# Performance work log

Hardware: AMD Instinct MI355X
Metric: run time of the kernel (lower is better)

## Reference

```python
import jax, jax.numpy as jnp
import numpy as np

N, OBS, H, M, L = 512, 32, 128, 128, 3


def _w(key, shape, fan_in):
    return jax.random.normal(key, shape, dtype=jnp.float32) / np.sqrt(fan_in)


def setup_inputs() -> dict:
    key = jax.random.key(0)
    ks = iter(jax.random.split(key, 64))
    inp = {}
    inp["obs"] = jax.random.normal(next(ks), (N, OBS), dtype=jnp.float32)
    inp["pos"] = jax.random.uniform(next(ks), (N, 2), dtype=jnp.float32)
    # encoder: obs_dim -> H -> H -> H
    inp["enc_W1"] = _w(next(ks), (H, OBS), OBS); inp["enc_b1"] = jnp.zeros((H,), jnp.float32)
    inp["enc_W2"] = _w(next(ks), (H, H), H);     inp["enc_b2"] = jnp.zeros((H,), jnp.float32)
    inp["enc_W3"] = _w(next(ks), (H, H), H);     inp["enc_b3"] = jnp.zeros((H,), jnp.float32)
    # per-layer message MLPs: (2H+1) -> M -> M -> M, stacked over L layers
    inp["msg_W1"] = _w(next(ks), (L, M, 2 * H + 1), 2 * H + 1); inp["msg_b1"] = jnp.zeros((L, M), jnp.float32)
    inp["msg_W2"] = _w(next(ks), (L, M, M), M);                 inp["msg_b2"] = jnp.zeros((L, M), jnp.float32)
    inp["msg_W3"] = _w(next(ks), (L, M, M), M);                 inp["msg_b3"] = jnp.zeros((L, M), jnp.float32)
    # per-layer update MLPs: (H+M) -> H -> H -> H, stacked over L layers
    inp["upd_W1"] = _w(next(ks), (L, H, H + M), H + M); inp["upd_b1"] = jnp.zeros((L, H), jnp.float32)
    inp["upd_W2"] = _w(next(ks), (L, H, H), H);         inp["upd_b2"] = jnp.zeros((L, H), jnp.float32)
    inp["upd_W3"] = _w(next(ks), (L, H, H), H);         inp["upd_b3"] = jnp.zeros((L, H), jnp.float32)
    return inp


def _mlp3(x, W1, b1, W2, b2, W3, b3):
    h = jax.nn.relu(x @ W1.T + b1)
    h = jax.nn.relu(h @ W2.T + b2)
    return h @ W3.T + b3


def reference(obs, pos, enc_W1, enc_b1, enc_W2, enc_b2, enc_W3, enc_b3,
              msg_W1, msg_b1, msg_W2, msg_b2, msg_W3, msg_b3,
              upd_W1, upd_b1, upd_W2, upd_b2, upd_W3, upd_b3):
    n = obs.shape[0]
    h = enc_W1.shape[0]
    z = _mlp3(obs, enc_W1, enc_b1, enc_W2, enc_b2, enc_W3, enc_b3)  # (N, H)
    # pairwise distances; guard diagonal sqrt(0) for grad safety, then zero it
    diff = pos[:, None, :] - pos[None, :, :]                  # (N, N, 2)
    sq = jnp.sum(diff * diff, axis=-1)                        # (N, N)
    eye = jnp.eye(n, dtype=pos.dtype)
    dist = jnp.sqrt(jnp.where(eye > 0, 1.0, sq)) * (1.0 - eye)
    nondiag = (1.0 - eye)[:, :, None]
    n_layers = msg_W1.shape[0]
    for l in range(n_layers):
        W1 = msg_W1[l]
        Wi, Wj, wd = W1[:, :h], W1[:, h:2 * h], W1[:, 2 * h]  # split concat [z_i, z_j, d]
        A = z @ Wi.T                                          # (N, M) receiver term
        B = z @ Wj.T                                          # (N, M) sender term
        h1 = jax.nn.relu(A[:, None, :] + B[None, :, :] + dist[:, :, None] * wd + msg_b1[l])  # (N, N, M)
        h2 = jax.nn.relu(jnp.einsum('ijm,km->ijk', h1, msg_W2[l]) + msg_b2[l])
        m = jnp.einsum('ijm,km->ijk', h2, msg_W3[l]) + msg_b3[l]
        m = m * nondiag                                       # exclude j == i
        msum = jnp.sum(m, axis=1)                             # (N, M) sum over senders j
        z = _mlp3(jnp.concatenate([z, msum], axis=-1),
                  upd_W1[l], upd_b1[l], upd_W2[l], upd_b2[l], upd_W3[l], upd_b3[l])
    return z
```

## Files before the change

kernel.cpp:

```cpp
#include <hip/hip_runtime.h>

#define NA 512
#define NOBS 32
#define NH 128

typedef const float* fp32p;
typedef __attribute__((ext_vector_type(8))) short bf16x8;
typedef __attribute__((ext_vector_type(4))) float f32x4;

__device__ __forceinline__ short f2bf(float f) {
    union { float f; unsigned u; } v; v.f = f;
    unsigned r = v.u + 0x7fffu + ((v.u >> 16) & 1u);
    return (short)(r >> 16);
}

__device__ __forceinline__ bf16x8 wfrag_f4(const float* p) {
    float4 u = *(const float4*)p;
    float4 v = *(const float4*)(p + 4);
    bf16x8 f;
    f[0] = f2bf(u.x); f[1] = f2bf(u.y); f[2] = f2bf(u.z); f[3] = f2bf(u.w);
    f[4] = f2bf(v.x); f[5] = f2bf(v.y); f[6] = f2bf(v.z); f[7] = f2bf(v.w);
    return f;
}

#define HSTR 136

__global__ __launch_bounds__(512) void enc_ab_kernel(
    fp32p obs, fp32p eW1, fp32p eb1, fp32p eW2, fp32p eb2, fp32p eW3, fp32p eb3,
    fp32p mW1, float* __restrict__ z, float* __restrict__ A, float* __restrict__ B) {
    const int i = blockIdx.x;
    const int t = threadIdx.x;
    const int nn = t >> 2;
    const int ks = t & 3;

    __shared__ float xs0[NOBS];
    __shared__ float part[4 * NH];
    __shared__ float part2[4 * NH];
    __shared__ float hx[NH], hy[NH], zz[NH];

    if (t < NOBS) xs0[t] = obs[(size_t)i * NOBS + t];
    __syncthreads();
    {
        const float* wr = eW1 + (size_t)nn * NOBS + ks * 8;
        const float4 w0 = *(const float4*)wr;
        const float4 w1 = *(const float4*)(wr + 4);
        const float4 x0 = *(const float4*)&xs0[ks * 8];
        const float4 x1 = *(const float4*)&xs0[ks * 8 + 4];
        part[ks * NH + nn] = w0.x * x0.x + w0.y * x0.y + w0.z * x0.z + w0.w * x0.w +
                             w1.x * x1.x + w1.y * x1.y + w1.z * x1.z + w1.w * x1.w;
    }
    __syncthreads();
    if (t < NH)
        hx[t] = fmaxf(eb1[t] + part[t] + part[NH + t] + part[2 * NH + t] + part[3 * NH + t], 0.f);
    __syncthreads();
    {
        const float* wr = eW2 + (size_t)nn * NH + ks * 4;
        float p = 0.f;
        #pragma unroll
        for (int it = 0; it < 8; ++it) {
            const float4 wv = *(const float4*)(wr + it * 16);
            const float4 xv = *(const float4*)&hx[it * 16 + ks * 4];
            p += wv.x * xv.x + wv.y * xv.y + wv.z * xv.z + wv.w * xv.w;
        }
        part[ks * NH + nn] = p;
    }
    __syncthreads();
    if (t < NH)
        hy[t] = fmaxf(eb2[t] + part[t] + part[NH + t] + part[2 * NH + t] + part[3 * NH + t], 0.f);
    __syncthreads();
    {
        const float* wr = eW3 + (size_t)nn * NH + ks * 4;
        float p = 0.f;
        #pragma unroll
        for (int it = 0; it < 8; ++it) {
            const float4 wv = *(const float4*)(wr + it * 16);
            const float4 xv = *(const float4*)&hy[it * 16 + ks * 4];
            p += wv.x * xv.x + wv.y * xv.y + wv.z * xv.z + wv.w * xv.w;
        }
        part[ks * NH + nn] = p;
    }
    __syncthreads();
    if (t < NH) {
        const float v = eb3[t] + part[t] + part[NH + t] + part[2 * NH + t] + part[3 * NH + t];
        z[(size_t)i * NH + t] = v;
        zz[t] = v;
    }
    __syncthreads();
    {
        const float* pr = mW1 + (size_t)nn * 257;
        float pa = 0.f, pb = 0.f;
        #pragma unroll
        for (int it = 0; it < 8; ++it) {
            #pragma unroll
            for (int j = 0; j < 4; ++j) {
                const int k = it * 16 + ks * 4 + j;
                const float x = zz[k];
                pa += x * pr[k];
                pb += x * pr[NH + k];
            }
        }
        part[ks * NH + nn] = pa;
        part2[ks * NH + nn] = pb;
    }
    __syncthreads();
    if (t < NH) {
        A[(size_t)i * NH + t] = part[t] + part[NH + t] + part[2 * NH + t] + part[3 * NH + t];
        B[(size_t)i * NH + t] = part2[t] + part2[NH + t] + part2[2 * NH + t] + part2[3 * NH + t];
    }
}

__global__ __launch_bounds__(512) void msg_upd_kernel(
    const float* __restrict__ A, const float* __restrict__ B,
    fp32p pos, const float* __restrict__ zin,
    fp32p W1l, fp32p b1, fp32p W2, fp32p b2, fp32p W3, fp32p b3,
    fp32p uW1, fp32p ub1, fp32p uW2, fp32p ub2, fp32p uW3, fp32p ub3,
    fp32p msgW1n, int do_ab,
    float* __restrict__ zout, float* __restrict__ An, float* __restrict__ Bn) {
    const int i = blockIdx.x;
    const int t = threadIdx.x;
    const int lane = t & 63;
    const int w = t >> 6;
    const int q = lane >> 4;
    const int c = lane & 15;
    const int ncol = w * 16 + c;

    __shared__ short h1s[128 * HSTR];
    __shared__ short h2s[128 * HSTR];
    __shared__ float distrow[NA];
    __shared__ float amrow[NH];
    __shared__ float wdsr[NH];
    __shared__ float xs2[2 * NH];
    __shared__ float part[4 * NH];
    __shared__ float part2[4 * NH];
    __shared__ float hx[NH], hy[NH], hz[NH];

    if (t < NH) {
        amrow[t] = A[i * NH + t] + b1[t];
        wdsr[t]  = W1l[t * 257 + 256];
        xs2[t] = zin[(size_t)i * NH + t];
    }
    {
        const float2 pi = *(const float2*)&pos[2 * i];
        const float2 pj = *(const float2*)&pos[2 * t];
        const float dx = pi.x - pj.x, dy = pi.y - pj.y;
        const float s = dx * dx + dy * dy;
        distrow[t] = (t == i) ? 0.0f : sqrtf(s);
    }

    bf16x8 w2f[4], w3f[4];
    {
        const float* w2r = W2 + (size_t)ncol * NH + q * 8;
        const float* w3r = W3 + (size_t)ncol * NH + q * 8;
        #pragma unroll
        for (int kb = 0; kb < 4; ++kb) {
            w2f[kb] = wfrag_f4(w2r + kb * 32);
            w3f[kb] = wfrag_f4(w3r + kb * 32);
        }
    }
    const float b2n = b2[ncol];
    const float b3n = b3[ncol];

    const int m2 = lane * 2;
    float psum = 0.0f;

    for (int c4 = 0; c4 < 4; ++c4) {
        const int j0 = c4 * 128;
        __syncthreads();

        {
            const float am0 = amrow[m2],     am1 = amrow[m2 + 1];
            const float wd0 = wdsr[m2],      wd1 = wdsr[m2 + 1];
            #pragma unroll
            for (int rr = 0; rr < 16; ++rr) {
                const int row = rr * 8 + w;
                const int jg  = j0 + row;
                const float2 bv = *(const float2*)&B[(size_t)jg * NH + m2];
                const float d = distrow[jg];
                const float v0 = fmaxf(am0 + bv.x + d * wd0, 0.0f);
                const float v1 = fmaxf(am1 + bv.y + d * wd1, 0.0f);
                const unsigned p = (unsigned)(unsigned short)f2bf(v0) |
                                   ((unsigned)(unsigned short)f2bf(v1) << 16);
                *(unsigned*)&h1s[row * HSTR + m2] = p;
            }
        }
        __syncthreads();

        #pragma unroll
        for (int jt = 0; jt < 8; ++jt) {
            f32x4 acc = {0.f, 0.f, 0.f, 0.f};
            const short* arow = &h1s[(jt * 16 + c) * HSTR + q * 8];
            #pragma unroll
            for (int kb = 0; kb < 4; ++kb) {
                bf16x8 a = *(const bf16x8*)(arow + kb * 32);
                acc = __builtin_amdgcn_mfma_f32_16x16x32_bf16(a, w2f[kb], acc, 0, 0, 0);
            }
            #pragma unroll
            for (int r = 0; r < 4; ++r) {
                const int row = jt * 16 + q * 4 + r;
                h2s[row * HSTR + ncol] = f2bf(fmaxf(acc[r] + b2n, 0.0f));
            }
        }
        __syncthreads();

        #pragma unroll
        for (int jt = 0; jt < 8; ++jt) {
            f32x4 acc = {0.f, 0.f, 0.f, 0.f};
            const short* arow = &h2s[(jt * 16 + c) * HSTR + q * 8];
            #pragma unroll
            for (int kb = 0; kb < 4; ++kb) {
                bf16x8 a = *(const bf16x8*)(arow + kb * 32);
                acc = __builtin_amdgcn_mfma_f32_16x16x32_bf16(a, w3f[kb], acc, 0, 0, 0);
            }
            #pragma unroll
            for (int r = 0; r < 4; ++r) {
                const int jg = j0 + jt * 16 + q * 4 + r;
                if (jg != i) psum += acc[r] + b3n;
            }
        }
    }

    psum += __shfl_xor(psum, 16, 64);
    psum += __shfl_xor(psum, 32, 64);
    if (lane < 16) xs2[NH + ncol] = psum;
    __syncthreads();

    const int nn = t >> 2;
    const int ks = t & 3;
    {
        const float* wr = uW1 + (size_t)nn * 256 + ks * 4;
        float p = 0.f;
        #pragma unroll
        for (int it = 0; it < 16; ++it) {
            const float4 wv = *(const float4*)(wr + it * 16);
            const float4 xv = *(const float4*)&xs2[it * 16 + ks * 4];
            p += wv.x * xv.x + wv.y * xv.y + wv.z * xv.z + wv.w * xv.w;
        }
        part[ks * NH + nn] = p;
    }
    __syncthreads();
    if (t < NH)
        hx[t] = fmaxf(ub1[t] + part[t] + part[NH + t] + part[2 * NH + t] + part[3 * NH + t], 0.f);
    __syncthreads();
    {
        const float* wr = uW2 + (size_t)nn * NH + ks * 4;
        float p = 0.f;
        #pragma unroll
        for (int it = 0; it < 8; ++it) {
            const float4 wv = *(const float4*)(wr + it * 16);
            const float4 xv = *(const float4*)&hx[it * 16 + ks * 4];
            p += wv.x * xv.x + wv.y * xv.y + wv.z * xv.z + wv.w * xv.w;
        }
        part[ks * NH + nn] = p;
    }
    __syncthreads();
    if (t < NH)
        hy[t] = fmaxf(ub2[t] + part[t] + part[NH + t] + part[2 * NH + t] + part[3 * NH + t], 0.f);
    __syncthreads();
    {
        const float* wr = uW3 + (size_t)nn * NH + ks * 4;
        float p = 0.f;
        #pragma unroll
        for (int it = 0; it < 8; ++it) {
            const float4 wv = *(const float4*)(wr + it * 16);
            const float4 xv = *(const float4*)&hy[it * 16 + ks * 4];
            p += wv.x * xv.x + wv.y * xv.y + wv.z * xv.z + wv.w * xv.w;
        }
        part[ks * NH + nn] = p;
    }
    __syncthreads();
    if (t < NH) {
        const float v = ub3[t] + part[t] + part[NH + t] + part[2 * NH + t] + part[3 * NH + t];
        zout[(size_t)i * NH + t] = v;
        hz[t] = v;
    }
    if (!do_ab) return;
    __syncthreads();
    {
        const float* pr = msgW1n + (size_t)nn * 257;
        float pa = 0.f, pb = 0.f;
        #pragma unroll
        for (int it = 0; it < 8; ++it) {
            #pragma unroll
            for (int j = 0; j < 4; ++j) {
                const int k = it * 16 + ks * 4 + j;
                const float x = hz[k];
                pa += x * pr[k];
                pb += x * pr[NH + k];
            }
        }
        part[ks * NH + nn] = pa;
        part2[ks * NH + nn] = pb;
    }
    __syncthreads();
    if (t < NH) {
        An[(size_t)i * NH + t] = part[t] + part[NH + t] + part[2 * NH + t] + part[3 * NH + t];
        Bn[(size_t)i * NH + t] = part2[t] + part2[NH + t] + part2[2 * NH + t] + part2[3 * NH + t];
    }
}

extern "C" void kernel_launch(void* const* d_in, const int* in_sizes, int n_in,
                              void* d_out, int out_size, void* d_ws, size_t ws_size,
                              hipStream_t stream) {
    fp32p obs   = (fp32p)d_in[0];
    fp32p pos   = (fp32p)d_in[1];
    fp32p encW1 = (fp32p)d_in[2];  fp32p encb1 = (fp32p)d_in[3];
    fp32p encW2 = (fp32p)d_in[4];  fp32p encb2 = (fp32p)d_in[5];
    fp32p encW3 = (fp32p)d_in[6];  fp32p encb3 = (fp32p)d_in[7];
    fp32p msgW1 = (fp32p)d_in[8];  fp32p msgb1 = (fp32p)d_in[9];
    fp32p msgW2 = (fp32p)d_in[10]; fp32p msgb2 = (fp32p)d_in[11];
    fp32p msgW3 = (fp32p)d_in[12]; fp32p msgb3 = (fp32p)d_in[13];
    fp32p updW1 = (fp32p)d_in[14]; fp32p updb1 = (fp32p)d_in[15];
    fp32p updW2 = (fp32p)d_in[16]; fp32p updb2 = (fp32p)d_in[17];
    fp32p updW3 = (fp32p)d_in[18]; fp32p updb3 = (fp32p)d_in[19];

    float* ws = (float*)d_ws;
    float* zA = ws;
    float* zB = zA + NA * NH;
    float* A0 = zB + NA * NH;
    float* B0 = A0 + NA * NH;
    float* A1 = B0 + NA * NH;
    float* B1 = A1 + NA * NH;

    enc_ab_kernel<<<NA, 512, 0, stream>>>(obs, encW1, encb1, encW2, encb2,
                                          encW3, encb3, msgW1, zA, A0, B0);

    float* zin = zA;  float* zout = zB;
    float* Ac = A0;   float* Bc = B0;
    float* An = A1;   float* Bn = B1;
    for (int l = 0; l < 3; ++l) {
        const int do_ab = (l < 2);
        float* dst = (l == 2) ? (float*)d_out : zout;
        msg_upd_kernel<<<NA, 512, 0, stream>>>(Ac, Bc, pos, zin,
            msgW1 + (size_t)l * 128 * 257, msgb1 + l * 128,
            msgW2 + (size_t)l * 128 * 128, msgb2 + l * 128,
            msgW3 + (size_t)l * 128 * 128, msgb3 + l * 128,
            updW1 + (size_t)l * 256 * 128, updb1 + l * 128,
            updW2 + (size_t)l * 128 * 128, updb2 + l * 128,
            updW3 + (size_t)l * 128 * 128, updb3 + l * 128,
            msgW1 + (size_t)(l + 1 < 3 ? l + 1 : 0) * 128 * 257, do_ab,
            dst, An, Bn);
        float* tmp;
        tmp = zin; zin = zout; zout = tmp;
        tmp = Ac; Ac = An; An = tmp;
        tmp = Bc; Bc = Bn; Bn = tmp;
    }
}
```

Baseline: 225.3 us.

## Fuse encoder and all message layers into one persistent kernel with grid barriers

Replaces the four separate kernel launches with a single persistent kernel that runs the encoder and all three message/update layers, using atomic-counter grid barriers between layers. The receiver term A and the node state z now stay in shared memory, and only B goes through global memory. The shared h1/h2 tiles shrink to 64 rows so that more blocks fit per CU and all 512 blocks can be co-resident. The barrier relies on every block being resident at once, so it could deadlock or serialise if occupancy is insufficient, and it adds spin-wait overhead.

```diff
diff --git a/kernel.cpp b/kernel.cpp
--- a/kernel.cpp
+++ b/kernel.cpp
@@ -25,19 +25,60 @@
 
 #define HSTR 136
 
-__global__ __launch_bounds__(512) void enc_ab_kernel(
-    fp32p obs, fp32p eW1, fp32p eb1, fp32p eW2, fp32p eb2, fp32p eW3, fp32p eb3,
-    fp32p mW1, float* __restrict__ z, float* __restrict__ A, float* __restrict__ B) {
+__device__ __forceinline__ void gsync(unsigned* cnt, int s) {
+    __threadfence();
+    __syncthreads();
+    if (threadIdx.x == 0) {
+        atomicAdd(&cnt[s], 1u);
+        while (__hip_atomic_load(&cnt[s], __ATOMIC_RELAXED,
+                                 __HIP_MEMORY_SCOPE_AGENT) < (unsigned)NA) {
+            __builtin_amdgcn_s_sleep(2);
+        }
+    }
+    __syncthreads();
+    (void)__hip_atomic_load(&cnt[s], __ATOMIC_ACQUIRE, __HIP_MEMORY_SCOPE_AGENT);
+}
+
+__global__ void init_kernel(unsigned* cnt) {
+    if (threadIdx.x < 8) cnt[threadIdx.x] = 0u;
+}
+
+__global__ __launch_bounds__(512) void gnn_kernel(
+    fp32p obs, fp32p pos,
+    fp32p eW1, fp32p eb1, fp32p eW2, fp32p eb2, fp32p eW3, fp32p eb3,
+    fp32p mW1, fp32p mb1, fp32p mW2, fp32p mb2, fp32p mW3, fp32p mb3,
+    fp32p uW1, fp32p ub1, fp32p uW2, fp32p ub2, fp32p uW3, fp32p ub3,
+    float* __restrict__ out, float* __restrict__ B0, float* __restrict__ B1,
+    unsigned* __restrict__ cnt) {
     const int i = blockIdx.x;
     const int t = threadIdx.x;
+    const int lane = t & 63;
+    const int w = t >> 6;
+    const int q = lane >> 4;
+    const int c = lane & 15;
+    const int ncol = w * 16 + c;
     const int nn = t >> 2;
     const int ks = t & 3;
 
-    __shared__ float xs0[NOBS];
+    __shared__ short h1s[64 * HSTR];
+    __shared__ short h2s[64 * HSTR];
+    __shared__ float distrow[NA];
+    __shared__ float amrow[NH];
+    __shared__ float wdsr[NH];
+    __shared__ float arow_s[NH];
+    __shared__ float xs2[2 * NH];
     __shared__ float part[4 * NH];
     __shared__ float part2[4 * NH];
-    __shared__ float hx[NH], hy[NH], zz[NH];
-
+    __shared__ float hx[NH], hy[NH];
+    __shared__ float xs0[NOBS];
+
+    {
+        const float2 pi = *(const float2*)&pos[2 * i];
+        const float2 pj = *(const float2*)&pos[2 * t];
+        const float dx = pi.x - pj.x, dy = pi.y - pj.y;
+        const float s = dx * dx + dy * dy;
+        distrow[t] = (t == i) ? 0.0f : sqrtf(s);
+    }
     if (t < NOBS) xs0[t] = obs[(size_t)i * NOBS + t];
     __syncthreads();
     {
@@ -80,11 +121,8 @@
         part[ks * NH + nn] = p;
     }
     __syncthreads();
-    if (t < NH) {
-        const float v = eb3[t] + part[t] + part[NH + t] + part[2 * NH + t] + part[3 * NH + t];
-        z[(size_t)i * NH + t] = v;
-        zz[t] = v;
-    }
+    if (t < NH)
+        xs2[t] = eb3[t] + part[t] + part[NH + t] + part[2 * NH + t] + part[3 * NH + t];
     __syncthreads();
     {
         const float* pr = mW1 + (size_t)nn * 257;
@@ -94,7 +132,7 @@
             #pragma unroll
             for (int j = 0; j < 4; ++j) {
                 const int k = it * 16 + ks * 4 + j;
-                const float x = zz[k];
+                const float x = xs2[k];
                 pa += x * pr[k];
                 pb += x * pr[NH + k];
             }
@@ -104,197 +142,181 @@
     }
     __syncthreads();
     if (t < NH) {
-        A[(size_t)i * NH + t] = part[t] + part[NH + t] + part[2 * NH + t] + part[3 * NH + t];
-        B[(size_t)i * NH + t] = part2[t] + part2[NH + t] + part2[2 * NH + t] + part2[3 * NH + t];
-    }
-}
-
-__global__ __launch_bounds__(512) void msg_upd_kernel(
-    const float* __restrict__ A, const float* __restrict__ B,
-    fp32p pos, const float* __restrict__ zin,
-    fp32p W1l, fp32p b1, fp32p W2, fp32p b2, fp32p W3, fp32p b3,
-    fp32p uW1, fp32p ub1, fp32p uW2, fp32p ub2, fp32p uW3, fp32p ub3,
-    fp32p msgW1n, int do_ab,
-    float* __restrict__ zout, float* __restrict__ An, float* __restrict__ Bn) {
-    const int i = blockIdx.x;
-    const int t = threadIdx.x;
-    const int lane = t & 63;
-    const int w = t >> 6;
-    const int q = lane >> 4;
-    const int c = lane & 15;
-    const int ncol = w * 16 + c;
-
-    __shared__ short h1s[128 * HSTR];
-    __shared__ short h2s[128 * HSTR];
-    __shared__ float distrow[NA];
-    __shared__ float amrow[NH];
-    __shared__ float wdsr[NH];
-    __shared__ float xs2[2 * NH];
-    __shared__ float part[4 * NH];
-    __shared__ float part2[4 * NH];
-    __shared__ float hx[NH], hy[NH], hz[NH];
-
-    if (t < NH) {
-        amrow[t] = A[i * NH + t] + b1[t];
-        wdsr[t]  = W1l[t * 257 + 256];
-        xs2[t] = zin[(size_t)i * NH + t];
-    }
-    {
-        const float2 pi = *(const float2*)&pos[2 * i];
-        const float2 pj = *(const float2*)&pos[2 * t];
-        const float dx = pi.x - pj.x, dy = pi.y - pj.y;
-        const float s = dx * dx + dy * dy;
-        distrow[t] = (t == i) ? 0.0f : sqrtf(s);
-    }
-
-    bf16x8 w2f[4], w3f[4];
-    {
-        const float* w2r = W2 + (size_t)ncol * NH + q * 8;
-        const float* w3r = W3 + (size_t)ncol * NH + q * 8;
-        #pragma unroll
-        for (int kb = 0; kb < 4; ++kb) {
-            w2f[kb] = wfrag_f4(w2r + kb * 32);
-            w3f[kb] = wfrag_f4(w3r + kb * 32);
-        }
-    }
-    const float b2n = b2[ncol];
-    const float b3n = b3[ncol];
-
-    const int m2 = lane * 2;
-    float psum = 0.0f;
-
-    for (int c4 = 0; c4 < 4; ++c4) {
-        const int j0 = c4 * 128;
-        __syncthreads();
-
+        arow_s[t] = part[t] + part[NH + t] + part[2 * NH + t] + part[3 * NH + t];
+        B0[(size_t)i * NH + t] = part2[t] + part2[NH + t] + part2[2 * NH + t] + part2[3 * NH + t];
+    }
+    gsync(cnt, 0);
+
+    for (int l = 0; l < 3; ++l) {
+        const float* Bc = (l == 1) ? B1 : B0;
+        float* Bn = (l == 0) ? B1 : B0;
+        fp32p W1l = mW1 + (size_t)l * 128 * 257;
+        fp32p b1l = mb1 + l * 128;
+        fp32p W2l = mW2 + (size_t)l * 128 * 128;
+        fp32p b2l = mb2 + l * 128;
+        fp32p W3l = mW3 + (size_t)l * 128 * 128;
+        fp32p b3l = mb3 + l * 128;
+        fp32p uW1l = uW1 + (size_t)l * 256 * 128;
+        fp32p ub1l = ub1 + l * 128;
+        fp32p uW2l = uW2 + (size_t)l * 128 * 128;
+        fp32p ub2l = ub2 + l * 128;
+        fp32p uW3l = uW3 + (size_t)l * 128 * 128;
+        fp32p ub3l = ub3 + l * 128;
+
+        if (t < NH) {
+            amrow[t] = arow_s[t] + b1l[t];
+            wdsr[t]  = W1l[t * 257 + 256];
+        }
+        bf16x8 w2f[4], w3f[4];
         {
-            const float am0 = amrow[m2],     am1 = amrow[m2 + 1];
-            const float wd0 = wdsr[m2],      wd1 = wdsr[m2 + 1];
-            #pragma unroll
-            for (int rr = 0; rr < 16; ++rr) {
-                const int row = rr * 8 + w;
-                const int jg  = j0 + row;
-                const float2 bv = *(const float2*)&B[(size_t)jg * NH + m2];
-                const float d = distrow[jg];
-                const float v0 = fmaxf(am0 + bv.x + d * wd0, 0.0f);
-                const float v1 = fmaxf(am1 + bv.y + d * wd1, 0.0f);
-                const unsigned p = (unsigned)(unsigned short)f2bf(v0) |
-                                   ((unsigned)(unsigned short)f2bf(v1) << 16);
-                *(unsigned*)&h1s[row * HSTR + m2] = p;
-            }
-        }
-        __syncthreads();
-
-        #pragma unroll
-        for (int jt = 0; jt < 8; ++jt) {
-            f32x4 acc = {0.f, 0.f, 0.f, 0.f};
-            const short* arow = &h1s[(jt * 16 + c) * HSTR + q * 8];
+            const float* w2r = W2l + (size_t)ncol * NH + q * 8;
+            const float* w3r = W3l + (size_t)ncol * NH + q * 8;
             #pragma unroll
             for (int kb = 0; kb < 4; ++kb) {
-                bf16x8 a = *(const bf16x8*)(arow + kb * 32);
-                acc = __builtin_amdgcn_mfma_f32_16x16x32_bf16(a, w2f[kb], acc, 0, 0, 0);
-            }
-            #pragma unroll
-            for (int r = 0; r < 4; ++r) {
-                const int row = jt * 16 + q * 4 + r;
-                h2s[row * HSTR + ncol] = f2bf(fmaxf(acc[r] + b2n, 0.0f));
-            }
-        }
-        __syncthreads();
-
-        #pragma unroll
-        for (int jt = 0; jt < 8; ++jt) {
-            f32x4 acc = {0.f, 0.f, 0.f, 0.f};
-            const short* arow = &h2s[(jt * 16 + c) * HSTR + q * 8];
-            #pragma unroll
-            for (int kb = 0; kb < 4; ++kb) {
-                bf16x8 a = *(const bf16x8*)(arow + kb * 32);
-                acc = __builtin_amdgcn_mfma_f32_16x16x32_bf16(a, w3f[kb], acc, 0, 0, 0);
-            }
-            #pragma unroll
-            for (int r = 0; r < 4; ++r) {
-                const int jg = j0 + jt * 16 + q * 4 + r;
-                if (jg != i) psum += acc[r] + b3n;
-            }
-        }
-    }
-
-    psum += __shfl_xor(psum, 16, 64);
-    psum += __shfl_xor(psum, 32, 64);
-    if (lane < 16) xs2[NH + ncol] = psum;
-    __syncthreads();
-
-    const int nn = t >> 2;
-    const int ks = t & 3;
-    {
-        const float* wr = uW1 + (size_t)nn * 256 + ks * 4;
-        float p = 0.f;
-        #pragma unroll
-        for (int it = 0; it < 16; ++it) {
-            const float4 wv = *(const float4*)(wr + it * 16);
-            const float4 xv = *(const float4*)&xs2[it * 16 + ks * 4];
-            p += wv.x * xv.x + wv.y * xv.y + wv.z * xv.z + wv.w * xv.w;
-        }
-        part[ks * NH + nn] = p;
-    }
-    __syncthreads();
-    if (t < NH)
-        hx[t] = fmaxf(ub1[t] + part[t] + part[NH + t] + part[2 * NH + t] + part[3 * NH + t], 0.f);
-    __syncthreads();
-    {
-        const float* wr = uW2 + (size_t)nn * NH + ks * 4;
-        float p = 0.f;
-        #pragma unroll
-        for (int it = 0; it < 8; ++it) {
-            const float4 wv = *(const float4*)(wr + it * 16);
-            const float4 xv = *(const float4*)&hx[it * 16 + ks * 4];
-            p += wv.x * xv.x + wv.y * xv.y + wv.z * xv.z + wv.w * xv.w;
-        }
-        part[ks * NH + nn] = p;
-    }
-    __syncthreads();
-    if (t < NH)
-        hy[t] = fmaxf(ub2[t] + part[t] + part[NH + t] + part[2 * NH + t] + part[3 * NH + t], 0.f);
-    __syncthreads();
-    {
-        const float* wr = uW3 + (size_t)nn * NH + ks * 4;
-        float p = 0.f;
-        #pragma unroll
-        for (int it = 0; it < 8; ++it) {
-            const float4 wv = *(const float4*)(wr + it * 16);
-            const float4 xv = *(const float4*)&hy[it * 16 + ks * 4];
-            p += wv.x * xv.x + wv.y * xv.y + wv.z * xv.z + wv.w * xv.w;
-        }
-        part[ks * NH + nn] = p;
-    }
-    __syncthreads();
-    if (t < NH) {
-        const float v = ub3[t] + part[t] + part[NH + t] + part[2 * NH + t] + part[3 * NH + t];
-        zout[(size_t)i * NH + t] = v;
-        hz[t] = v;
-    }
-    if (!do_ab) return;
-    __syncthreads();
-    {
-        const float* pr = msgW1n + (size_t)nn * 257;
-        float pa = 0.f, pb = 0.f;
-        #pragma unroll
-        for (int it = 0; it < 8; ++it) {
-            #pragma unroll
-            for (int j = 0; j < 4; ++j) {
-                const int k = it * 16 + ks * 4 + j;
-                const float x = hz[k];
-                pa += x * pr[k];
-                pb += x * pr[NH + k];
-            }
-        }
-        part[ks * NH + nn] = pa;
-        part2[ks * NH + nn] = pb;
-    }
-    __syncthreads();
-    if (t < NH) {
-        An[(size_t)i * NH + t] = part[t] + part[NH + t] + part[2 * NH + t] + part[3 * NH + t];
-        Bn[(size_t)i * NH + t] = part2[t] + part2[NH + t] + part2[2 * NH + t] + part2[3 * NH + t];
+                w2f[kb] = wfrag_f4(w2r + kb * 32);
+                w3f[kb] = wfrag_f4(w3r + kb * 32);
+            }
+        }
+        const float b2n = b2l[ncol];
+        const float b3n = b3l[ncol];
+
+        const int m2 = lane * 2;
+        float psum = 0.0f;
+
+        for (int c8 = 0; c8 < 8; ++c8) {
+            const int j0 = c8 * 64;
+            __syncthreads();
+
+            {
+                const float am0 = amrow[m2],     am1 = amrow[m2 + 1];
+                const float wd0 = wdsr[m2],      wd1 = wdsr[m2 + 1];
+                #pragma unroll
+                for (int rr = 0; rr < 8; ++rr) {
+                    const int row = rr * 8 + w;
+                    const int jg  = j0 + row;
+                    const float2 bv = *(const float2*)&Bc[(size_t)jg * NH + m2];
+                    const float d = distrow[jg];
+                    const float v0 = fmaxf(am0 + bv.x + d * wd0, 0.0f);
+                    const float v1 = fmaxf(am1 + bv.y + d * wd1, 0.0f);
+                    const unsigned p = (unsigned)(unsigned short)f2bf(v0) |
+                                       ((unsigned)(unsigned short)f2bf(v1) << 16);
+                    *(unsigned*)&h1s[row * HSTR + m2] = p;
+                }
+            }
+            __syncthreads();
+
+            #pragma unroll
+            for (int jt = 0; jt < 4; ++jt) {
+                f32x4 acc = {0.f, 0.f, 0.f, 0.f};
+                const short* arow = &h1s[(jt * 16 + c) * HSTR + q * 8];
+                #pragma unroll
+                for (int kb = 0; kb < 4; ++kb) {
+                    bf16x8 a = *(const bf16x8*)(arow + kb * 32);
+                    acc = __builtin_amdgcn_mfma_f32_16x16x32_bf16(a, w2f[kb], acc, 0, 0, 0);
+                }
+                #pragma unroll
+                for (int r = 0; r < 4; ++r) {
+                    const int row = jt * 16 + q * 4 + r;
+                    h2s[row * HSTR + ncol] = f2bf(fmaxf(acc[r] + b2n, 0.0f));
+                }
+            }
+            __syncthreads();
+
+            #pragma unroll
+            for (int jt = 0; jt < 4; ++jt) {
+                f32x4 acc = {0.f, 0.f, 0.f, 0.f};
+                const short* arow = &h2s[(jt * 16 + c) * HSTR + q * 8];
+                #pragma unroll
+                for (int kb = 0; kb < 4; ++kb) {
+                    bf16x8 a = *(const bf16x8*)(arow + kb * 32);
+                    acc = __builtin_amdgcn_mfma_f32_16x16x32_bf16(a, w3f[kb], acc, 0, 0, 0);
+                }
+                #pragma unroll
+                for (int r = 0; r < 4; ++r) {
+                    const int jg = j0 + jt * 16 + q * 4 + r;
+                    if (jg != i) psum += acc[r] + b3n;
+                }
+            }
+        }
+
+        psum += __shfl_xor(psum, 16, 64);
+        psum += __shfl_xor(psum, 32, 64);
+        if (lane < 16) xs2[NH + ncol] = psum;
+        __syncthreads();
+
+        {
+            const float* wr = uW1l + (size_t)nn * 256 + ks * 4;
+            float p = 0.f;
+            #pragma unroll
+            for (int it = 0; it < 16; ++it) {
+                const float4 wv = *(const float4*)(wr + it * 16);
+                const float4 xv = *(const float4*)&xs2[it * 16 + ks * 4];
+                p += wv.x * xv.x + wv.y * xv.y + wv.z * xv.z + wv.w * xv.w;
+            }
+            part[ks * NH + nn] = p;
+        }
+        __syncthreads();
+        if (t < NH)
+            hx[t] = fmaxf(ub1l[t] + part[t] + part[NH + t] + part[2 * NH + t] + part[3 * NH + t], 0.f);
+        __syncthreads();
+        {
+            const float* wr = uW2l + (size_t)nn * NH + ks * 4;
+            float p = 0.f;
+            #pragma unroll
+            for (int it = 0; it < 8; ++it) {
+                const float4 wv = *(const float4*)(wr + it * 16);
+                const float4 xv = *(const float4*)&hx[it * 16 + ks * 4];
+                p += wv.x * xv.x + wv.y * xv.y + wv.z * xv.z + wv.w * xv.w;
+            }
+            part[ks * NH + nn] = p;
+        }
+        __syncthreads();
+        if (t < NH)
+            hy[t] = fmaxf(ub2l[t] + part[t] + part[NH + t] + part[2 * NH + t] + part[3 * NH + t], 0.f);
+        __syncthreads();
+        {
+            const float* wr = uW3l + (size_t)nn * NH + ks * 4;
+            float p = 0.f;
+            #pragma unroll
+            for (int it = 0; it < 8; ++it) {
+                const float4 wv = *(const float4*)(wr + it * 16);
+                const float4 xv = *(const float4*)&hy[it * 16 + ks * 4];
+                p += wv.x * xv.x + wv.y * xv.y + wv.z * xv.z + wv.w * xv.w;
+            }
+            part[ks * NH + nn] = p;
+        }
+        __syncthreads();
+        if (t < NH) {
+            const float v = ub3l[t] + part[t] + part[NH + t] + part[2 * NH + t] + part[3 * NH + t];
+            if (l == 2) out[(size_t)i * NH + t] = v;
+            hx[t] = v;
+        }
+        if (l < 2) {
+            __syncthreads();
+            {
+                const float* pr = mW1 + (size_t)(l + 1) * 128 * 257 + (size_t)nn * 257;
+                float pa = 0.f, pb = 0.f;
+                #pragma unroll
+                for (int it = 0; it < 8; ++it) {
+                    #pragma unroll
+                    for (int j = 0; j < 4; ++j) {
+                        const int k = it * 16 + ks * 4 + j;
+                        const float x = hx[k];
+                        pa += x * pr[k];
+                        pb += x * pr[NH + k];
+                    }
+                }
+                part[ks * NH + nn] = pa;
+                part2[ks * NH + nn] = pb;
+            }
+            __syncthreads();
+            if (t < NH) {
+                arow_s[t] = part[t] + part[NH + t] + part[2 * NH + t] + part[3 * NH + t];
+                Bn[(size_t)i * NH + t] = part2[t] + part2[NH + t] + part2[2 * NH + t] + part2[3 * NH + t];
+                xs2[t] = hx[t];
+            }
+            gsync(cnt, 1 + l);
+        }
     }
 }
 
@@ -314,34 +336,15 @@
     fp32p updW3 = (fp32p)d_in[18]; fp32p updb3 = (fp32p)d_in[19];
 
     float* ws = (float*)d_ws;
-    float* zA = ws;
-    float* zB = zA + NA * NH;
-    float* A0 = zB + NA * NH;
-    float* B0 = A0 + NA * NH;
-    float* A1 = B0 + NA * NH;
-    float* B1 = A1 + NA * NH;
-
-    enc_ab_kernel<<<NA, 512, 0, stream>>>(obs, encW1, encb1, encW2, encb2,
-                                          encW3, encb3, msgW1, zA, A0, B0);
-
-    float* zin = zA;  float* zout = zB;
-    float* Ac = A0;   float* Bc = B0;
-    float* An = A1;   float* Bn = B1;
-    for (int l = 0; l < 3; ++l) {
-        const int do_ab = (l < 2);
-        float* dst = (l == 2) ? (float*)d_out : zout;
-        msg_upd_kernel<<<NA, 512, 0, stream>>>(Ac, Bc, pos, zin,
-            msgW1 + (size_t)l * 128 * 257, msgb1 + l * 128,
-            msgW2 + (size_t)l * 128 * 128, msgb2 + l * 128,
-            msgW3 + (size_t)l * 128 * 128, msgb3 + l * 128,
-            updW1 + (size_t)l * 256 * 128, updb1 + l * 128,
-            updW2 + (size_t)l * 128 * 128, updb2 + l * 128,
-            updW3 + (size_t)l * 128 * 128, updb3 + l * 128,
-            msgW1 + (size_t)(l + 1 < 3 ? l + 1 : 0) * 128 * 257, do_ab,
-            dst, An, Bn);
-        float* tmp;
-        tmp = zin; zin = zout; zout = tmp;
-        tmp = Ac; Ac = An; An = tmp;
-        tmp = Bc; Bc = Bn; Bn = tmp;
-    }
-}
+    float* B0 = ws;
+    float* B1 = B0 + NA * NH;
+    unsigned* cnt = (unsigned*)(B1 + NA * NH);
+
+    init_kernel<<<1, 64, 0, stream>>>(cnt);
+    gnn_kernel<<<NA, 512, 0, stream>>>(
+        obs, pos,
+        encW1, encb1, encW2, encb2, encW3, encb3,
+        msgW1, msgb1, msgW2, msgb2, msgW3, msgb3,
+        updW1, updb1, updW2, updb2, updW3, updb3,
+        (float*)d_out, B0, B1, cnt);
+}
```

Result: slower. 597.5 us (+165.2%).

## Split each node's sender loop across two blocks with atomic last-block tail

Applied to the files above, without the earlier changes.

Each message/update kernel now launches two blocks per receiver node, each handling half of the senders with half-sized LDS tiles. Partial message sums go to a global scratch buffer, and an atomic counter picks the last-arriving block, which combines the halves and runs the update MLP. The aim is to double the grid (1024 blocks instead of 512) and cut LDS per block so more blocks fit per CU on the many-CU GPU. The cost is an extra counter-init kernel, global round-trips for the partial sums, and atomic synchronization, and the update tail now runs in only half the blocks.

```diff
diff --git a/kernel.cpp b/kernel.cpp
--- a/kernel.cpp
+++ b/kernel.cpp
@@ -25,6 +25,10 @@
 
 #define HSTR 136
 
+__global__ void init_kernel(unsigned* tcnt) {
+    tcnt[blockIdx.x * 512 + threadIdx.x] = 0u;
+}
+
 __global__ __launch_bounds__(512) void enc_ab_kernel(
     fp32p obs, fp32p eW1, fp32p eb1, fp32p eW2, fp32p eb2, fp32p eW3, fp32p eb3,
     fp32p mW1, float* __restrict__ z, float* __restrict__ A, float* __restrict__ B) {
@@ -115,8 +119,11 @@
     fp32p W1l, fp32p b1, fp32p W2, fp32p b2, fp32p W3, fp32p b3,
     fp32p uW1, fp32p ub1, fp32p uW2, fp32p ub2, fp32p uW3, fp32p ub3,
     fp32p msgW1n, int do_ab,
-    float* __restrict__ zout, float* __restrict__ An, float* __restrict__ Bn) {
-    const int i = blockIdx.x;
+    float* __restrict__ zout, float* __restrict__ An, float* __restrict__ Bn,
+    float* __restrict__ mpart, unsigned* __restrict__ tcnt) {
+    const int bid = blockIdx.x;
+    const int i = bid >> 1;
+    const int half = bid & 1;
     const int t = threadIdx.x;
     const int lane = t & 63;
     const int w = t >> 6;
@@ -124,20 +131,17 @@
     const int c = lane & 15;
     const int ncol = w * 16 + c;
 
-    __shared__ short h1s[128 * HSTR];
-    __shared__ short h2s[128 * HSTR];
+    __shared__ short h1s[64 * HSTR];
+    __shared__ short h2s[64 * HSTR];
     __shared__ float distrow[NA];
     __shared__ float amrow[NH];
     __shared__ float wdsr[NH];
-    __shared__ float xs2[2 * NH];
-    __shared__ float part[4 * NH];
-    __shared__ float part2[4 * NH];
-    __shared__ float hx[NH], hy[NH], hz[NH];
+    __shared__ float msum_s[NH];
+    __shared__ int tail_flag;
 
     if (t < NH) {
         amrow[t] = A[i * NH + t] + b1[t];
         wdsr[t]  = W1l[t * 257 + 256];
-        xs2[t] = zin[(size_t)i * NH + t];
     }
     {
         const float2 pi = *(const float2*)&pos[2 * i];
@@ -163,15 +167,15 @@
     const int m2 = lane * 2;
     float psum = 0.0f;
 
-    for (int c4 = 0; c4 < 4; ++c4) {
-        const int j0 = c4 * 128;
+    for (int c8 = half * 4; c8 < half * 4 + 4; ++c8) {
+        const int j0 = c8 * 64;
         __syncthreads();
 
         {
             const float am0 = amrow[m2],     am1 = amrow[m2 + 1];
             const float wd0 = wdsr[m2],      wd1 = wdsr[m2 + 1];
             #pragma unroll
-            for (int rr = 0; rr < 16; ++rr) {
+            for (int rr = 0; rr < 8; ++rr) {
                 const int row = rr * 8 + w;
                 const int jg  = j0 + row;
                 const float2 bv = *(const float2*)&B[(size_t)jg * NH + m2];
@@ -186,7 +190,7 @@
         __syncthreads();
 
         #pragma unroll
-        for (int jt = 0; jt < 8; ++jt) {
+        for (int jt = 0; jt < 4; ++jt) {
             f32x4 acc = {0.f, 0.f, 0.f, 0.f};
             const short* arow = &h1s[(jt * 16 + c) * HSTR + q * 8];
             #pragma unroll
@@ -203,7 +207,7 @@
         __syncthreads();
 
         #pragma unroll
-        for (int jt = 0; jt < 8; ++jt) {
+        for (int jt = 0; jt < 4; ++jt) {
             f32x4 acc = {0.f, 0.f, 0.f, 0.f};
             const short* arow = &h2s[(jt * 16 + c) * HSTR + q * 8];
             #pragma unroll
@@ -221,7 +225,35 @@
 
     psum += __shfl_xor(psum, 16, 64);
     psum += __shfl_xor(psum, 32, 64);
-    if (lane < 16) xs2[NH + ncol] = psum;
+    if (lane < 16) msum_s[ncol] = psum;
+    __syncthreads();
+    if (t < NH)
+        __hip_atomic_store(&mpart[((size_t)half * NA + i) * NH + t], msum_s[t],
+                           __ATOMIC_RELAXED, __HIP_MEMORY_SCOPE_AGENT);
+    __syncthreads();
+    if (t == 0) {
+        unsigned old = __hip_atomic_fetch_add(&tcnt[i], 1u, __ATOMIC_ACQ_REL,
+                                              __HIP_MEMORY_SCOPE_AGENT);
+        tail_flag = (old == 1u) ? 1 : 0;
+    }
+    __syncthreads();
+    if (!tail_flag) return;
+
+    float* pool  = (float*)h1s;
+    float* xs2   = pool;
+    float* part  = pool + 256;
+    float* part2 = pool + 768;
+    float* hx    = pool + 1280;
+    float* hy    = pool + 1408;
+    float* hz    = pool + 1536;
+    if (t < NH) {
+        const float m0 = __hip_atomic_load(&mpart[(size_t)i * NH + t],
+                                           __ATOMIC_RELAXED, __HIP_MEMORY_SCOPE_AGENT);
+        const float m1 = __hip_atomic_load(&mpart[((size_t)NA + i) * NH + t],
+                                           __ATOMIC_RELAXED, __HIP_MEMORY_SCOPE_AGENT);
+        xs2[t] = zin[(size_t)i * NH + t];
+        xs2[NH + t] = m0 + m1;
+    }
     __syncthreads();
 
     const int nn = t >> 2;
@@ -320,7 +352,10 @@
     float* B0 = A0 + NA * NH;
     float* A1 = B0 + NA * NH;
     float* B1 = A1 + NA * NH;
-
+    float* mpart = B1 + NA * NH;
+    unsigned* tcnt = (unsigned*)(mpart + 2 * NA * NH);
+
+    init_kernel<<<3, 512, 0, stream>>>(tcnt);
     enc_ab_kernel<<<NA, 512, 0, stream>>>(obs, encW1, encb1, encW2, encb2,
                                           encW3, encb3, msgW1, zA, A0, B0);
 
@@ -330,7 +365,7 @@
     for (int l = 0; l < 3; ++l) {
         const int do_ab = (l < 2);
         float* dst = (l == 2) ? (float*)d_out : zout;
-        msg_upd_kernel<<<NA, 512, 0, stream>>>(Ac, Bc, pos, zin,
+        msg_upd_kernel<<<NA * 2, 512, 0, stream>>>(Ac, Bc, pos, zin,
             msgW1 + (size_t)l * 128 * 257, msgb1 + l * 128,
             msgW2 + (size_t)l * 128 * 128, msgb2 + l * 128,
             msgW3 + (size_t)l * 128 * 128, msgb3 + l * 128,
@@ -338,7 +373,7 @@
             updW2 + (size_t)l * 128 * 128, updb2 + l * 128,
             updW3 + (size_t)l * 128 * 128, updb3 + l * 128,
             msgW1 + (size_t)(l + 1 < 3 ? l + 1 : 0) * 128 * 257, do_ab,
-            dst, An, Bn);
+            dst, An, Bn, mpart, tcnt + l * NA);
         float* tmp;
         tmp = zin; zin = zout; zout = tmp;
         tmp = Ac; Ac = An; An = tmp;
```

New measurement: 299.5 us. 32.9% more time.
